# Optimization experiments

Hardware: AMD Instinct MI355X
Metric: run time of the kernel (lower is better)

Reference implementation:

```python
import jax, jax.numpy as jnp
import numpy as np

N, D = 4096, 1024

def setup_inputs() -> dict:
    key = jax.random.key(0)
    k0, k1, k2, k3 = jax.random.split(key, 4)
    s = 1.0 / np.sqrt(D)
    return {
        "x": jax.random.normal(k0, (N, D), dtype=jnp.float32),
        "Wq": jax.random.normal(k1, (D, N), dtype=jnp.float32) * s,
        "Wk": jax.random.normal(k2, (D, N), dtype=jnp.float32) * s,
        "Wv": jax.random.normal(k3, (D, N), dtype=jnp.float32) * s,
    }

def reference(x, Wq, Wk, Wv):
    # Projections: (N, D) @ (D, N) -> (N, N)
    q = x @ Wq
    k = x @ Wk
    v = x @ Wv
    # score[i, j] = q_i . k_j  -> softmax over axis=1 (per query row)
    score = q @ k.T                      # (N, N)
    p = jax.nn.softmax(score, axis=1)    # (N, N)
    # Original: sum_i v[i, :] * softmax(score)^T[i, j]  == p @ v  (N, N)
    # (the broadcast outer-product+sum is mathematically a matmul)
    return p @ v
```

## Files before the change

### kernel.cpp

```cpp
#include <hip/hip_runtime.h>
#include <hip/hip_bf16.h>
#include <stdint.h>

typedef __attribute__((ext_vector_type(8))) short short8v;
typedef __attribute__((ext_vector_type(8))) _Float16 half8v;
typedef __attribute__((ext_vector_type(4))) float f32x4;

__device__ __forceinline__ unsigned short f2bf(float f) {
  unsigned u = __builtin_bit_cast(unsigned, f);
  unsigned r = 0x7fffu + ((u >> 16) & 1u);
  return (unsigned short)((u + r) >> 16);
}
__device__ __forceinline__ float bf2f(unsigned short h) {
  unsigned u = ((unsigned)h) << 16;
  return __builtin_bit_cast(float, u);
}
__device__ __forceinline__ unsigned short f2h(float f) {
  _Float16 h = (_Float16)f;
  return __builtin_bit_cast(unsigned short, h);
}
__device__ __forceinline__ void gload_lds16(const void* g, void* l) {
  __builtin_amdgcn_global_load_lds(
      (const __attribute__((address_space(1))) void*)g,
      (__attribute__((address_space(3))) void*)l, 16, 0, 0);
}
#define SBAR  __builtin_amdgcn_s_barrier()
#define SCHED __builtin_amdgcn_sched_barrier(0)

__global__ __launch_bounds__(256) void split_plain(
    const float4* __restrict__ X, ushort4* __restrict__ H, ushort4* __restrict__ L, int n4) {
  int idx = blockIdx.x * 256 + threadIdx.x;
  if (idx >= n4) return;
  float4 v = X[idx];
  ushort4 h, l;
  h.x = f2bf(v.x); l.x = f2bf(v.x - bf2f(h.x));
  h.y = f2bf(v.y); l.y = f2bf(v.y - bf2f(h.y));
  h.z = f2bf(v.z); l.z = f2bf(v.z - bf2f(h.z));
  h.w = f2bf(v.w); l.w = f2bf(v.w - bf2f(h.w));
  H[idx] = h; L[idx] = l;
}

__global__ __launch_bounds__(256) void tof16_plain(
    const float4* __restrict__ X, ushort4* __restrict__ H, int n4) {
  int idx = blockIdx.x * 256 + threadIdx.x;
  if (idx >= n4) return;
  float4 v = X[idx];
  ushort4 h;
  h.x = f2h(v.x); h.y = f2h(v.y); h.z = f2h(v.z); h.w = f2h(v.w);
  H[idx] = h;
}

__global__ __launch_bounds__(256) void split_T(
    const float* __restrict__ W, unsigned short* __restrict__ H,
    unsigned short* __restrict__ L, int Kd, int Nd) {
  __shared__ float tile[32][33];
  const int t = threadIdx.x;
  const int c = t & 31;
  const int r0 = t >> 5;
  const int k0 = blockIdx.y * 32, n0 = blockIdx.x * 32;
#pragma unroll
  for (int i = 0; i < 4; ++i) {
    int r = r0 + i * 8;
    tile[r][c] = W[(size_t)(k0 + r) * Nd + n0 + c];
  }
  __syncthreads();
#pragma unroll
  for (int i = 0; i < 4; ++i) {
    int n = r0 + i * 8;
    float f = tile[c][n];
    unsigned short h = f2bf(f);
    unsigned short l = f2bf(f - bf2f(h));
    size_t o = (size_t)(n0 + n) * Kd + k0 + c;
    H[o] = h; L[o] = l;
  }
}

__global__ __launch_bounds__(256) void reduceT_M(
    const float* __restrict__ P, unsigned short* __restrict__ H,
    unsigned short* __restrict__ L, int nsplit) {
  __shared__ float tile[32][33];
  const int t = threadIdx.x;
  const int c = t & 31;
  const int r0 = t >> 5;
  const int a0 = blockIdx.y * 32, b0 = blockIdx.x * 32;
#pragma unroll
  for (int i = 0; i < 4; ++i) {
    int r = r0 + i * 8;
    float s = 0.f;
    for (int sp = 0; sp < nsplit; ++sp)
      s += P[(size_t)sp * 1048576 + (size_t)(a0 + r) * 1024 + b0 + c];
    tile[r][c] = s;
  }
  __syncthreads();
#pragma unroll
  for (int i = 0; i < 4; ++i) {
    int b = r0 + i * 8;
    float f = tile[c][b];
    unsigned short h = f2bf(f);
    size_t o = (size_t)(b0 + b) * 1024 + a0 + c;
    H[o] = h;
    L[o] = f2bf(f - bf2f(h));
  }
}

__global__ __launch_bounds__(256) void reduce_split(
    const float4* __restrict__ P, ushort4* __restrict__ H, ushort4* __restrict__ L,
    int n4, int nsplit, int stride4) {
  int idx = blockIdx.x * 256 + threadIdx.x;
  if (idx >= n4) return;
  float4 s = P[idx];
  for (int sp = 1; sp < nsplit; ++sp) {
    float4 v = P[(size_t)sp * stride4 + idx];
    s.x += v.x; s.y += v.y; s.z += v.z; s.w += v.w;
  }
  ushort4 h, l;
  h.x = f2bf(s.x); l.x = f2bf(s.x - bf2f(h.x));
  h.y = f2bf(s.y); l.y = f2bf(s.y - bf2f(h.y));
  h.z = f2bf(s.z); l.z = f2bf(s.z - bf2f(h.z));
  h.w = f2bf(s.w); l.w = f2bf(s.w - bf2f(h.w));
  H[idx] = h; L[idx] = l;
}

__global__ __launch_bounds__(256) void reduce_f16(
    const float4* __restrict__ P, ushort4* __restrict__ H,
    int n4, int nsplit, int stride4) {
  int idx = blockIdx.x * 256 + threadIdx.x;
  if (idx >= n4) return;
  float4 s = P[idx];
  for (int sp = 1; sp < nsplit; ++sp) {
    float4 v = P[(size_t)sp * stride4 + idx];
    s.x += v.x; s.y += v.y; s.z += v.z; s.w += v.w;
  }
  ushort4 h;
  h.x = f2h(s.x); h.y = f2h(s.y); h.z = f2h(s.z); h.w = f2h(s.w);
  H[idx] = h;
}

template<bool SWZ>
__global__ __launch_bounds__(512, 1) void gemm_fused3(
    const unsigned short* __restrict__ base,
    unsigned dAh, unsigned dAl, unsigned dBh, unsigned dBl,
    int N, int K, int kchunk, int tilesX,
    float* __restrict__ Cf, size_t partStride) {
  __shared__ unsigned short lds[65536];
  const int AH = 0, BH = 8192, BL = 16384, AL = 24576;
  const int NT = kchunk >> 5;
  const int wg = blockIdx.x;
  int bx, by;
  if (SWZ) { const int sw = ((wg & 7) << 5) | (wg >> 3); bx = sw & 15; by = sw >> 4; }
  else     { bx = wg % tilesX; by = wg / tilesX; }
  const int m0 = by << 8, n0 = bx << 8;
  const unsigned koff = (unsigned)blockIdx.y * (unsigned)kchunk;
  Cf += (size_t)blockIdx.y * partStride;

  const int tid = threadIdx.x;
  const int w = tid >> 6, lane = tid & 63;
  const int wr = w >> 2, wc = w & 3;
  const int lr = lane & 15;
  const int phys = (lane >> 4) ^ ((lr >> 1) & 3);
  const int aoff = (wr * 128 + lr) * 32 + phys * 8;
  const int boff = (wc * 64 + lr) * 32 + phys * 8;
  const int rst = tid >> 2;
  const int ssrc = ((tid & 3) ^ ((tid >> 3) & 3)) * 8;
  const unsigned jstep = 128u * (unsigned)K;

  const unsigned voffA = (unsigned)(m0 + rst) * (unsigned)K + (unsigned)ssrc + koff;
  const unsigned voffB = (unsigned)(n0 + rst) * (unsigned)K + (unsigned)ssrc + koff;

  f32x4 acc[8][4];
#pragma unroll
  for (int m = 0; m < 8; ++m)
#pragma unroll
    for (int n = 0; n < 4; ++n) acc[m][n] = {0.f, 0.f, 0.f, 0.f};

#define STG2(dsel, vo, loff, s, tt) do {                                     \
    const unsigned o_ = (vo) + (dsel) + (unsigned)(tt) * 32u;                \
    gload_lds16(base + o_,         &lds[(s) + (loff) + (w << 9)]);           \
    gload_lds16(base + o_ + jstep, &lds[(s) + (loff) + 4096 + (w << 9)]);    \
  } while (0)

  STG2(dAh, voffA, AH, 0, 0);
  STG2(dBl, voffB, BL, 0, 0);
  STG2(dBh, voffB, BH, 0, 0);
  STG2(dAl, voffA, AL, 0, 0);

  for (int t = 0; t < NT; ++t) {
    const int slot = (t & 1) << 15;
    const int slot1 = ((t + 1) & 1) << 15;
    const bool st = (t + 1) < NT;
    short8v ahf[8];
    SCHED; asm volatile("s_waitcnt vmcnt(4)"); SBAR; SCHED;
    {
      short8v bf[4];
#pragma unroll
      for (int n = 0; n < 4; ++n)
        bf[n] = *(const short8v*)&lds[slot + BL + boff + n * 512];
#pragma unroll
      for (int m = 0; m < 8; ++m)
        ahf[m] = *(const short8v*)&lds[slot + AH + aoff + m * 512];
      if (st) { STG2(dAh, voffA, AH, slot1, t + 1); STG2(dBl, voffB, BL, slot1, t + 1); }
      __builtin_amdgcn_s_setprio(1);
#pragma unroll
      for (int m = 0; m < 8; ++m)
#pragma unroll
        for (int n = 0; n < 4; ++n)
          acc[m][n] = __builtin_amdgcn_mfma_f32_16x16x32_bf16(ahf[m], bf[n], acc[m][n], 0, 0, 0);
      __builtin_amdgcn_s_setprio(0);
    }
    SCHED;
    if (st) { asm volatile("s_waitcnt vmcnt(6)"); }
    else    { asm volatile("s_waitcnt vmcnt(2)"); }
    SBAR; SCHED;
    short8v bh[4];
    {
#pragma unroll
      for (int n = 0; n < 4; ++n)
        bh[n] = *(const short8v*)&lds[slot + BH + boff + n * 512];
      if (st) { STG2(dBh, voffB, BH, slot1, t + 1); }
      __builtin_amdgcn_s_setprio(1);
#pragma unroll
      for (int m = 0; m < 8; ++m)
#pragma unroll
        for (int n = 0; n < 4; ++n)
          acc[m][n] = __builtin_amdgcn_mfma_f32_16x16x32_bf16(ahf[m], bh[n], acc[m][n], 0, 0, 0);
      __builtin_amdgcn_s_setprio(0);
    }
    SCHED;
    if (st) { asm volatile("s_waitcnt vmcnt(6)"); }
    else    { asm volatile("s_waitcnt vmcnt(0)"); }
    SBAR; SCHED;
    {
      short8v alf[8];
#pragma unroll
      for (int m = 0; m < 8; ++m)
        alf[m] = *(const short8v*)&lds[slot + AL + aoff + m * 512];
      if (st) { STG2(dAl, voffA, AL, slot1, t + 1); }
      __builtin_amdgcn_s_setprio(1);
#pragma unroll
      for (int m = 0; m < 8; ++m)
#pragma unroll
        for (int n = 0; n < 4; ++n)
          acc[m][n] = __builtin_amdgcn_mfma_f32_16x16x32_bf16(alf[m], bh[n], acc[m][n], 0, 0, 0);
      __builtin_amdgcn_s_setprio(0);
    }
    SCHED;
  }
#undef STG2

  const int crow = m0 + wr * 128 + ((lane >> 4) << 2);
  const int ccol = n0 + wc * 64 + lr;
#pragma unroll
  for (int mi = 0; mi < 8; ++mi)
#pragma unroll
    for (int r = 0; r < 4; ++r) {
      const int row = crow + mi * 16 + r;
#pragma unroll
      for (int n = 0; n < 4; ++n)
        Cf[(size_t)row * N + ccol + n * 16] = acc[mi][n][r];
    }
}

template<int EPI, bool SWZ, int DT>
__global__ __launch_bounds__(512, 2) void gemm_plain(
    const unsigned short* __restrict__ A, const unsigned short* __restrict__ B,
    int N, int K, int kchunk, int tilesX,
    float* __restrict__ Cf, unsigned short* __restrict__ Ch, size_t partStride) {
  __shared__ unsigned short lds[65536];
  const int NT = kchunk >> 5;
  const int wg = blockIdx.x;
  int bx, by;
  if (SWZ) { const int sw = ((wg & 7) << 5) | (wg >> 3); bx = sw & 15; by = sw >> 4; }
  else     { bx = wg % tilesX; by = wg / tilesX; }
  const int m0 = by << 8, n0 = bx << 8;
  const unsigned koff = (unsigned)blockIdx.y * (unsigned)kchunk;
  Cf += (size_t)blockIdx.y * partStride;

  const int tid = threadIdx.x;
  const int w = tid >> 6, lane = tid & 63;
  const int wr = w >> 2, wc = w & 3;
  const int lr = lane & 15;
  const int phys = (lane >> 4) ^ ((lr >> 1) & 3);
  const int aoff = (wr * 128 + lr) * 32 + phys * 8;
  const int boff = 8192 + (wc * 64 + lr) * 32 + phys * 8;
  const int rst = w * 16 + (lane >> 2);
  const int ssrc = ((lane & 3) ^ ((lane >> 3) & 3)) * 8;

  f32x4 acc[8][4];
#pragma unroll
  for (int m = 0; m < 8; ++m)
#pragma unroll
    for (int n = 0; n < 4; ++n) acc[m][n] = {0.f, 0.f, 0.f, 0.f};

  const unsigned short* gA = A + (size_t)(m0 + rst) * K + ssrc + koff;
  const unsigned short* gB = B + (size_t)(n0 + rst) * K + ssrc + koff;
  const size_t jstep = (size_t)128 * K;

#define MFMA_DT(af, bf, c) (DT == 1 ? \
    __builtin_amdgcn_mfma_f32_16x16x32_f16(__builtin_bit_cast(half8v, af), \
        __builtin_bit_cast(half8v, bf), (c), 0, 0, 0) : \
    __builtin_amdgcn_mfma_f32_16x16x32_bf16((af), (bf), (c), 0, 0, 0))

#pragma unroll
  for (int tau = 0; tau < 3; ++tau) {
    const int so = tau * 16384 + (w << 9);
    gload_lds16(gA + (size_t)tau * 32, &lds[so]);
    gload_lds16(gA + (size_t)tau * 32 + jstep, &lds[so + 4096]);
    gload_lds16(gB + (size_t)tau * 32, &lds[so + 8192]);
    gload_lds16(gB + (size_t)tau * 32 + jstep, &lds[so + 12288]);
  }
  asm volatile("s_waitcnt vmcnt(8)");
  SCHED; SBAR; SCHED;

  for (int t = 0; t < NT; ++t) {
    const int sb = (t & 3) * 16384;
    if (t + 3 < NT) {
      const int so = ((t + 3) & 3) * 16384 + (w << 9);
      const unsigned short* srcA = gA + (size_t)(t + 3) * 32;
      const unsigned short* srcB = gB + (size_t)(t + 3) * 32;
      gload_lds16(srcA, &lds[so]);
      gload_lds16(srcA + jstep, &lds[so + 4096]);
      gload_lds16(srcB, &lds[so + 8192]);
      gload_lds16(srcB + jstep, &lds[so + 12288]);
    }
    short8v bfr[4], af0[4], af1[4];
#pragma unroll
    for (int n = 0; n < 4; ++n)
      bfr[n] = *(const short8v*)&lds[sb + boff + n * 512];
#pragma unroll
    for (int m = 0; m < 4; ++m)
      af0[m] = *(const short8v*)&lds[sb + aoff + m * 512];
#pragma unroll
    for (int m = 0; m < 4; ++m)
      af1[m] = *(const short8v*)&lds[sb + aoff + 2048 + m * 512];
    __builtin_amdgcn_s_setprio(1);
#pragma unroll
    for (int m = 0; m < 4; ++m)
#pragma unroll
      for (int n = 0; n < 4; ++n)
        acc[m][n] = MFMA_DT(af0[m], bfr[n], acc[m][n]);
#pragma unroll
    for (int m = 0; m < 4; ++m)
#pragma unroll
      for (int n = 0; n < 4; ++n)
        acc[4 + m][n] = MFMA_DT(af1[m], bfr[n], acc[4 + m][n]);
    __builtin_amdgcn_s_setprio(0);
    SCHED;
    if (t < NT - 3)       { asm volatile("s_waitcnt vmcnt(8)"); }
    else if (t == NT - 3) { asm volatile("s_waitcnt vmcnt(4)"); }
    else if (t == NT - 2) { asm volatile("s_waitcnt vmcnt(0)"); }
    SCHED;
    if (t < NT - 1) { SBAR; SCHED; }
  }
#undef MFMA_DT

  const int crow = m0 + wr * 128 + ((lane >> 4) << 2);
  const int ccol = n0 + wc * 64 + lr;
#pragma unroll
  for (int mi = 0; mi < 8; ++mi)
#pragma unroll
    for (int r = 0; r < 4; ++r) {
      const int row = crow + mi * 16 + r;
#pragma unroll
      for (int n = 0; n < 4; ++n) {
        const int col = ccol + n * 16;
        const float f = acc[mi][n][r];
        const size_t o = (size_t)row * N + col;
        if (EPI == 0) Cf[o] = f;
        else          Ch[o] = f2bf(f);
      }
    }
}

__global__ __launch_bounds__(256) void softmax_rows(
    const float* __restrict__ S, unsigned short* __restrict__ P, int n) {
  const int row = blockIdx.x;
  const int t = threadIdx.x;
  const float4* src = (const float4*)(S + (size_t)row * n);
  float4 v[4];
  float mx = -3.0e38f;
#pragma unroll
  for (int i = 0; i < 4; ++i) {
    v[i] = src[i * 256 + t];
    mx = fmaxf(mx, fmaxf(fmaxf(v[i].x, v[i].y), fmaxf(v[i].z, v[i].w)));
  }
#pragma unroll
  for (int off = 32; off; off >>= 1) mx = fmaxf(mx, __shfl_xor(mx, off));
  __shared__ float redm[4], reds[4];
  const int wid = t >> 6, lane = t & 63;
  if (lane == 0) redm[wid] = mx;
  __syncthreads();
  mx = fmaxf(fmaxf(redm[0], redm[1]), fmaxf(redm[2], redm[3]));
  float sum = 0.f;
#pragma unroll
  for (int i = 0; i < 4; ++i) {
    v[i].x = __expf(v[i].x - mx);
    v[i].y = __expf(v[i].y - mx);
    v[i].z = __expf(v[i].z - mx);
    v[i].w = __expf(v[i].w - mx);
    sum += (v[i].x + v[i].y) + (v[i].z + v[i].w);
  }
#pragma unroll
  for (int off = 32; off; off >>= 1) sum += __shfl_xor(sum, off);
  if (lane == 0) reds[wid] = sum;
  __syncthreads();
  sum = (reds[0] + reds[1]) + (reds[2] + reds[3]);
  float inv = 1.0f / sum;
#pragma unroll
  for (int i = 0; i < 4; ++i) {
    ushort4 o;
    o.x = f2bf(v[i].x * inv);
    o.y = f2bf(v[i].y * inv);
    o.z = f2bf(v[i].z * inv);
    o.w = f2bf(v[i].w * inv);
    *(ushort4*)(P + (size_t)row * n + (size_t)(i * 256 + t) * 4) = o;
  }
}

extern "C" void kernel_launch(void* const* d_in, const int* in_sizes, int n_in,
                              void* d_out, int out_size, void* d_ws, size_t ws_size,
                              hipStream_t stream) {
  (void)in_sizes; (void)n_in; (void)out_size; (void)ws_size;
  const float* x  = (const float*)d_in[0];
  const float* Wq = (const float*)d_in[1];
  const float* Wk = (const float*)d_in[2];
  const float* Wv = (const float*)d_in[3];
  const int N = 4096, D = 1024;
  const size_t MB = 1ull << 20;
  const unsigned MEL = (unsigned)(MB / 2);
  char* ws = (char*)d_ws;
  unsigned short* xh  = (unsigned short*)(ws + 0 * MB);
  unsigned short* xl  = (unsigned short*)(ws + 8 * MB);
  unsigned short* wqh = (unsigned short*)(ws + 16 * MB);
  unsigned short* wql = (unsigned short*)(ws + 24 * MB);
  unsigned short* wkh = (unsigned short*)(ws + 32 * MB);
  unsigned short* wkl = (unsigned short*)(ws + 40 * MB);
  unsigned short* wvh = (unsigned short*)(ws + 48 * MB);
  unsigned short* Mth = (unsigned short*)(ws + 56 * MB);
  unsigned short* Mtl = (unsigned short*)(ws + 58 * MB);
  unsigned short* p   = (unsigned short*)(ws + 64 * MB);
  float*          Mpart = (float*)(ws + 96 * MB);
  float*          ypart = (float*)(ws + 96 * MB);
  float*          zpart = (float*)(ws + 96 * MB);
  unsigned short* y16 = (unsigned short*)(ws + 16 * MB);
  unsigned short* zh  = (unsigned short*)(ws + 32 * MB);
  unsigned short* zl  = (unsigned short*)(ws + 40 * MB);
  unsigned short* xTh = (unsigned short*)(ws + 160 * MB);
  unsigned short* xTl = (unsigned short*)(ws + 168 * MB);
  unsigned short* wvl = (unsigned short*)(ws + 176 * MB);
  unsigned short* x16 = (unsigned short*)(ws + 184 * MB);
  float* score = (float*)d_out;
  float* out   = (float*)d_out;

  split_plain<<<4096, 256, 0, stream>>>((const float4*)x,  (ushort4*)xh,  (ushort4*)xl,  1048576);
  split_plain<<<4096, 256, 0, stream>>>((const float4*)Wq, (ushort4*)wqh, (ushort4*)wql, 1048576);
  split_plain<<<4096, 256, 0, stream>>>((const float4*)Wk, (ushort4*)wkh, (ushort4*)wkl, 1048576);
  split_T<<<dim3(N / 32, D / 32), 256, 0, stream>>>(Wv, wvh, wvl, D, N);
  split_T<<<dim3(D / 32, N / 32), 256, 0, stream>>>(x, xTh, xTl, N, D);
  tof16_plain<<<4096, 256, 0, stream>>>((const float4*)x, (ushort4*)x16, 1048576);

  gemm_fused3<false><<<dim3(16, 16), 512, 0, stream>>>(
      wqh, 0u, 8 * MEL, 16 * MEL, 24 * MEL,
      1024, 4096, 256, 4, Mpart, (size_t)1024 * 1024);
  reduceT_M<<<dim3(32, 32), 256, 0, stream>>>(Mpart, Mth, Mtl, 16);

  gemm_fused3<false><<<dim3(64, 4), 512, 0, stream>>>(
      xh, 0u, 8 * MEL, 56 * MEL, 58 * MEL,
      1024, 1024, 256, 4, ypart, (size_t)4096 * 1024);
  reduce_f16<<<4096, 256, 0, stream>>>(
      (const float4*)ypart, (ushort4*)y16, 1048576, 4, 1048576);

  gemm_plain<0, true, 1><<<dim3(256, 1), 512, 0, stream>>>(
      y16, x16, N, 1024, 1024, 16, score, nullptr, 0);

  softmax_rows<<<N, 256, 0, stream>>>(score, p, N);

  gemm_plain<0, false, 0><<<dim3(64, 4), 512, 0, stream>>>(
      p, xTh, 1024, 4096, 1024, 4, zpart, nullptr, (size_t)4096 * 1024);
  reduce_split<<<4096, 256, 0, stream>>>(
      (const float4*)zpart, (ushort4*)zh, (ushort4*)zl, 1048576, 4, 1048576);

  gemm_plain<0, true, 0><<<256, 512, 0, stream>>>(
      zh, wvh, N, 1024, 1024, 16, out, nullptr, 0);
}
```

Measured before the change: 298.0 us.

## Shrink plain GEMM tiles to 128x128 and drop unused low-part conversions

Replaces the 256x256-tile, 512-thread plain GEMM with a 128x128-tile, 256-thread variant using half the LDS. This quadruples the workgroup count for the score, PV and output GEMMs so the device's compute units are better filled. It also fuses the x f16 conversion into the bf16 hi/lo split kernel and stops writing low-part bf16 buffers that the plain GEMMs never read (Wv, xT, z). Smaller tiles give less operand reuse per loaded byte and more global traffic in exchange for better occupancy and load balance.

```diff
diff --git a/kernel.cpp b/kernel.cpp
--- a/kernel.cpp
+++ b/kernel.cpp
@@ -40,16 +40,21 @@
   H[idx] = h; L[idx] = l;
 }
 
-__global__ __launch_bounds__(256) void tof16_plain(
-    const float4* __restrict__ X, ushort4* __restrict__ H, int n4) {
+__global__ __launch_bounds__(256) void split_x3(
+    const float4* __restrict__ X, ushort4* __restrict__ H, ushort4* __restrict__ L,
+    ushort4* __restrict__ F, int n4) {
   int idx = blockIdx.x * 256 + threadIdx.x;
   if (idx >= n4) return;
   float4 v = X[idx];
-  ushort4 h;
-  h.x = f2h(v.x); h.y = f2h(v.y); h.z = f2h(v.z); h.w = f2h(v.w);
-  H[idx] = h;
-}
-
+  ushort4 h, l, f;
+  h.x = f2bf(v.x); l.x = f2bf(v.x - bf2f(h.x)); f.x = f2h(v.x);
+  h.y = f2bf(v.y); l.y = f2bf(v.y - bf2f(h.y)); f.y = f2h(v.y);
+  h.z = f2bf(v.z); l.z = f2bf(v.z - bf2f(h.z)); f.z = f2h(v.z);
+  h.w = f2bf(v.w); l.w = f2bf(v.w - bf2f(h.w)); f.w = f2h(v.w);
+  H[idx] = h; L[idx] = l; F[idx] = f;
+}
+
+template<bool WL>
 __global__ __launch_bounds__(256) void split_T(
     const float* __restrict__ W, unsigned short* __restrict__ H,
     unsigned short* __restrict__ L, int Kd, int Nd) {
@@ -69,9 +74,9 @@
     int n = r0 + i * 8;
     float f = tile[c][n];
     unsigned short h = f2bf(f);
-    unsigned short l = f2bf(f - bf2f(h));
     size_t o = (size_t)(n0 + n) * Kd + k0 + c;
-    H[o] = h; L[o] = l;
+    H[o] = h;
+    if (WL) L[o] = f2bf(f - bf2f(h));
   }
 }
 
@@ -101,24 +106,6 @@
     H[o] = h;
     L[o] = f2bf(f - bf2f(h));
   }
-}
-
-__global__ __launch_bounds__(256) void reduce_split(
-    const float4* __restrict__ P, ushort4* __restrict__ H, ushort4* __restrict__ L,
-    int n4, int nsplit, int stride4) {
-  int idx = blockIdx.x * 256 + threadIdx.x;
-  if (idx >= n4) return;
-  float4 s = P[idx];
-  for (int sp = 1; sp < nsplit; ++sp) {
-    float4 v = P[(size_t)sp * stride4 + idx];
-    s.x += v.x; s.y += v.y; s.z += v.z; s.w += v.w;
-  }
-  ushort4 h, l;
-  h.x = f2bf(s.x); l.x = f2bf(s.x - bf2f(h.x));
-  h.y = f2bf(s.y); l.y = f2bf(s.y - bf2f(h.y));
-  h.z = f2bf(s.z); l.z = f2bf(s.z - bf2f(h.z));
-  h.w = f2bf(s.w); l.w = f2bf(s.w - bf2f(h.w));
-  H[idx] = h; L[idx] = l;
 }
 
 __global__ __launch_bounds__(256) void reduce_f16(
@@ -133,6 +120,21 @@
   }
   ushort4 h;
   h.x = f2h(s.x); h.y = f2h(s.y); h.z = f2h(s.z); h.w = f2h(s.w);
+  H[idx] = h;
+}
+
+__global__ __launch_bounds__(256) void reduce_bf16(
+    const float4* __restrict__ P, ushort4* __restrict__ H,
+    int n4, int nsplit, int stride4) {
+  int idx = blockIdx.x * 256 + threadIdx.x;
+  if (idx >= n4) return;
+  float4 s = P[idx];
+  for (int sp = 1; sp < nsplit; ++sp) {
+    float4 v = P[(size_t)sp * stride4 + idx];
+    s.x += v.x; s.y += v.y; s.z += v.z; s.w += v.w;
+  }
+  ushort4 h;
+  h.x = f2bf(s.x); h.y = f2bf(s.y); h.z = f2bf(s.z); h.w = f2bf(s.w);
   H[idx] = h;
 }
 
@@ -260,40 +262,40 @@
     }
 }
 
-template<int EPI, bool SWZ, int DT>
-__global__ __launch_bounds__(512, 2) void gemm_plain(
+template<bool SWZ, int DT>
+__global__ __launch_bounds__(256, 2) void gemm_plain128(
     const unsigned short* __restrict__ A, const unsigned short* __restrict__ B,
     int N, int K, int kchunk, int tilesX,
-    float* __restrict__ Cf, unsigned short* __restrict__ Ch, size_t partStride) {
-  __shared__ unsigned short lds[65536];
+    float* __restrict__ Cf, size_t partStride) {
+  __shared__ unsigned short lds[32768];
   const int NT = kchunk >> 5;
   const int wg = blockIdx.x;
   int bx, by;
-  if (SWZ) { const int sw = ((wg & 7) << 5) | (wg >> 3); bx = sw & 15; by = sw >> 4; }
+  if (SWZ) { const int sw = ((wg & 7) << 7) | (wg >> 3); bx = sw & 31; by = sw >> 5; }
   else     { bx = wg % tilesX; by = wg / tilesX; }
-  const int m0 = by << 8, n0 = bx << 8;
+  const int m0 = by << 7, n0 = bx << 7;
   const unsigned koff = (unsigned)blockIdx.y * (unsigned)kchunk;
   Cf += (size_t)blockIdx.y * partStride;
 
   const int tid = threadIdx.x;
   const int w = tid >> 6, lane = tid & 63;
-  const int wr = w >> 2, wc = w & 3;
+  const int wr = w >> 1, wc = w & 1;
   const int lr = lane & 15;
   const int phys = (lane >> 4) ^ ((lr >> 1) & 3);
-  const int aoff = (wr * 128 + lr) * 32 + phys * 8;
-  const int boff = 8192 + (wc * 64 + lr) * 32 + phys * 8;
+  const int aoff = (wr * 64 + lr) * 32 + phys * 8;
+  const int boff = 4096 + (wc * 64 + lr) * 32 + phys * 8;
   const int rst = w * 16 + (lane >> 2);
   const int ssrc = ((lane & 3) ^ ((lane >> 3) & 3)) * 8;
 
-  f32x4 acc[8][4];
-#pragma unroll
-  for (int m = 0; m < 8; ++m)
+  f32x4 acc[4][4];
+#pragma unroll
+  for (int m = 0; m < 4; ++m)
 #pragma unroll
     for (int n = 0; n < 4; ++n) acc[m][n] = {0.f, 0.f, 0.f, 0.f};
 
   const unsigned short* gA = A + (size_t)(m0 + rst) * K + ssrc + koff;
   const unsigned short* gB = B + (size_t)(n0 + rst) * K + ssrc + koff;
-  const size_t jstep = (size_t)128 * K;
+  const size_t jstep = (size_t)64 * K;
 
 #define MFMA_DT(af, bf, c) (DT == 1 ? \
     __builtin_amdgcn_mfma_f32_16x16x32_f16(__builtin_bit_cast(half8v, af), \
@@ -302,47 +304,39 @@
 
 #pragma unroll
   for (int tau = 0; tau < 3; ++tau) {
-    const int so = tau * 16384 + (w << 9);
+    const int so = tau * 8192 + (w << 9);
     gload_lds16(gA + (size_t)tau * 32, &lds[so]);
-    gload_lds16(gA + (size_t)tau * 32 + jstep, &lds[so + 4096]);
-    gload_lds16(gB + (size_t)tau * 32, &lds[so + 8192]);
-    gload_lds16(gB + (size_t)tau * 32 + jstep, &lds[so + 12288]);
+    gload_lds16(gA + (size_t)tau * 32 + jstep, &lds[so + 2048]);
+    gload_lds16(gB + (size_t)tau * 32, &lds[so + 4096]);
+    gload_lds16(gB + (size_t)tau * 32 + jstep, &lds[so + 6144]);
   }
   asm volatile("s_waitcnt vmcnt(8)");
   SCHED; SBAR; SCHED;
 
   for (int t = 0; t < NT; ++t) {
-    const int sb = (t & 3) * 16384;
+    const int sb = (t & 3) * 8192;
     if (t + 3 < NT) {
-      const int so = ((t + 3) & 3) * 16384 + (w << 9);
+      const int so = ((t + 3) & 3) * 8192 + (w << 9);
       const unsigned short* srcA = gA + (size_t)(t + 3) * 32;
       const unsigned short* srcB = gB + (size_t)(t + 3) * 32;
       gload_lds16(srcA, &lds[so]);
-      gload_lds16(srcA + jstep, &lds[so + 4096]);
-      gload_lds16(srcB, &lds[so + 8192]);
-      gload_lds16(srcB + jstep, &lds[so + 12288]);
-    }
-    short8v bfr[4], af0[4], af1[4];
+      gload_lds16(srcA + jstep, &lds[so + 2048]);
+      gload_lds16(srcB, &lds[so + 4096]);
+      gload_lds16(srcB + jstep, &lds[so + 6144]);
+    }
+    short8v bfr[4], af[4];
 #pragma unroll
     for (int n = 0; n < 4; ++n)
       bfr[n] = *(const short8v*)&lds[sb + boff + n * 512];
 #pragma unroll
     for (int m = 0; m < 4; ++m)
-      af0[m] = *(const short8v*)&lds[sb + aoff + m * 512];
+      af[m] = *(const short8v*)&lds[sb + aoff + m * 512];
+    __builtin_amdgcn_s_setprio(1);
 #pragma unroll
     for (int m = 0; m < 4; ++m)
-      af1[m] = *(const short8v*)&lds[sb + aoff + 2048 + m * 512];
-    __builtin_amdgcn_s_setprio(1);
-#pragma unroll
-    for (int m = 0; m < 4; ++m)
 #pragma unroll
       for (int n = 0; n < 4; ++n)
-        acc[m][n] = MFMA_DT(af0[m], bfr[n], acc[m][n]);
-#pragma unroll
-    for (int m = 0; m < 4; ++m)
-#pragma unroll
-      for (int n = 0; n < 4; ++n)
-        acc[4 + m][n] = MFMA_DT(af1[m], bfr[n], acc[4 + m][n]);
+        acc[m][n] = MFMA_DT(af[m], bfr[n], acc[m][n]);
     __builtin_amdgcn_s_setprio(0);
     SCHED;
     if (t < NT - 3)       { asm volatile("s_waitcnt vmcnt(8)"); }
@@ -353,21 +347,16 @@
   }
 #undef MFMA_DT
 
-  const int crow = m0 + wr * 128 + ((lane >> 4) << 2);
+  const int crow = m0 + wr * 64 + ((lane >> 4) << 2);
   const int ccol = n0 + wc * 64 + lr;
 #pragma unroll
-  for (int mi = 0; mi < 8; ++mi)
+  for (int mi = 0; mi < 4; ++mi)
 #pragma unroll
     for (int r = 0; r < 4; ++r) {
       const int row = crow + mi * 16 + r;
 #pragma unroll
-      for (int n = 0; n < 4; ++n) {
-        const int col = ccol + n * 16;
-        const float f = acc[mi][n][r];
-        const size_t o = (size_t)row * N + col;
-        if (EPI == 0) Cf[o] = f;
-        else          Ch[o] = f2bf(f);
-      }
+      for (int n = 0; n < 4; ++n)
+        Cf[(size_t)row * N + ccol + n * 16] = acc[mi][n][r];
     }
 }
 
@@ -443,20 +432,17 @@
   float*          zpart = (float*)(ws + 96 * MB);
   unsigned short* y16 = (unsigned short*)(ws + 16 * MB);
   unsigned short* zh  = (unsigned short*)(ws + 32 * MB);
-  unsigned short* zl  = (unsigned short*)(ws + 40 * MB);
   unsigned short* xTh = (unsigned short*)(ws + 160 * MB);
-  unsigned short* xTl = (unsigned short*)(ws + 168 * MB);
-  unsigned short* wvl = (unsigned short*)(ws + 176 * MB);
   unsigned short* x16 = (unsigned short*)(ws + 184 * MB);
   float* score = (float*)d_out;
   float* out   = (float*)d_out;
 
-  split_plain<<<4096, 256, 0, stream>>>((const float4*)x,  (ushort4*)xh,  (ushort4*)xl,  1048576);
+  split_x3<<<4096, 256, 0, stream>>>((const float4*)x, (ushort4*)xh, (ushort4*)xl,
+                                     (ushort4*)x16, 1048576);
   split_plain<<<4096, 256, 0, stream>>>((const float4*)Wq, (ushort4*)wqh, (ushort4*)wql, 1048576);
   split_plain<<<4096, 256, 0, stream>>>((const float4*)Wk, (ushort4*)wkh, (ushort4*)wkl, 1048576);
-  split_T<<<dim3(N / 32, D / 32), 256, 0, stream>>>(Wv, wvh, wvl, D, N);
-  split_T<<<dim3(D / 32, N / 32), 256, 0, stream>>>(x, xTh, xTl, N, D);
-  tof16_plain<<<4096, 256, 0, stream>>>((const float4*)x, (ushort4*)x16, 1048576);
+  split_T<false><<<dim3(N / 32, D / 32), 256, 0, stream>>>(Wv, wvh, nullptr, D, N);
+  split_T<false><<<dim3(D / 32, N / 32), 256, 0, stream>>>(x, xTh, nullptr, N, D);
 
   gemm_fused3<false><<<dim3(16, 16), 512, 0, stream>>>(
       wqh, 0u, 8 * MEL, 16 * MEL, 24 * MEL,
@@ -469,16 +455,16 @@
   reduce_f16<<<4096, 256, 0, stream>>>(
       (const float4*)ypart, (ushort4*)y16, 1048576, 4, 1048576);
 
-  gemm_plain<0, true, 1><<<dim3(256, 1), 512, 0, stream>>>(
-      y16, x16, N, 1024, 1024, 16, score, nullptr, 0);
+  gemm_plain128<true, 1><<<dim3(1024, 1), 256, 0, stream>>>(
+      y16, x16, N, 1024, 1024, 32, score, 0);
 
   softmax_rows<<<N, 256, 0, stream>>>(score, p, N);
 
-  gemm_plain<0, false, 0><<<dim3(64, 4), 512, 0, stream>>>(
-      p, xTh, 1024, 4096, 1024, 4, zpart, nullptr, (size_t)4096 * 1024);
-  reduce_split<<<4096, 256, 0, stream>>>(
-      (const float4*)zpart, (ushort4*)zh, (ushort4*)zl, 1048576, 4, 1048576);
-
-  gemm_plain<0, true, 0><<<256, 512, 0, stream>>>(
-      zh, wvh, N, 1024, 1024, 16, out, nullptr, 0);
-}
+  gemm_plain128<false, 0><<<dim3(256, 4), 256, 0, stream>>>(
+      p, xTh, 1024, 4096, 1024, 8, zpart, (size_t)4096 * 1024);
+  reduce_bf16<<<4096, 256, 0, stream>>>(
+      (const float4*)zpart, (ushort4*)zh, 1048576, 4, 1048576);
+
+  gemm_plain128<true, 0><<<dim3(1024, 1), 256, 0, stream>>>(
+      zh, wvh, N, 1024, 1024, 32, out, 0);
+}
```

Result: slower. 316.7 us (+6.3%).
